# Kernel optimization log

Hardware: AMD Instinct MI355X
Metric: run time of the kernel (lower is better)

The kernel has to match this reference:

```python
import jax, jax.numpy as jnp
import numpy as np

TW = 25; HID = 128; LAYERS = 6; SPATIAL = 1; NVAR = 1
TMAX = 4.0; TMIN = 0.0; RES_T = 250.0; DOM = 16.0
N = 65536; B = 8; E = 393216
EPS = 1e-5


def swish(x):
    return x * jax.nn.sigmoid(x)


def _forward(u, x_pos, t_pos, variables,
             emb_w1, emb_b1, emb_w2, emb_b2,
             m1_w, m1_b, m2_w, m2_b,
             u1_w, u1_b, u2_w, u2_b,
             c1_w, c1_b, c2_w, c2_b,
             edge_index, batch):
    t_norm = t_pos / TMAX                       # [N]
    pos = x_pos / DOM                           # [N, 1] normalized by domain extent
    node_in = jnp.concatenate([u, pos, t_norm[:, None], variables], axis=-1)
    f = swish(node_in @ emb_w1 + emb_b1)
    f = swish(f @ emb_w2 + emb_b2)              # [N, HID]

    var_all = jnp.concatenate([t_norm[:, None], variables], axis=-1)  # [N, NVAR+1]
    src, dst = edge_index[0], edge_index[1]     # PyG: x_j = x[src], x_i = x[dst]
    du = u[dst] - u[src]                        # [E, TW]
    dp = pos[dst] - pos[src]                    # [E, SPATIAL]
    v_i = var_all[dst]                          # [E, NVAR+1]

    ones_e = jnp.ones((E,), f.dtype)
    deg = jnp.maximum(jax.ops.segment_sum(ones_e, dst, num_segments=N), 1.0)
    ones_n = jnp.ones((N,), f.dtype)
    gcount = jnp.maximum(jax.ops.segment_sum(ones_n, batch, num_segments=B), 1.0)

    for l in range(LAYERS):
        # message: concat(x_i, x_j, u_i-u_j, pos_i-pos_j, vars_i) -> 2-layer MLP
        m = jnp.concatenate([f[dst], f[src], du, dp, v_i], axis=-1)  # [E, 284]
        m = swish(m @ m1_w[l] + m1_b[l])
        m = swish(m @ m2_w[l] + m2_b[l])
        agg = jax.ops.segment_sum(m, dst, num_segments=N) / deg[:, None]  # mean aggr
        # update: concat(x, message, vars) -> 2-layer MLP, residual (in==out)
        h = jnp.concatenate([f, agg, var_all], axis=-1)  # [N, 258]
        h = swish(h @ u1_w[l] + u1_b[l])
        h = swish(h @ u2_w[l] + u2_b[l])
        h = f + h
        # InstanceNorm over nodes within each graph, per feature (no affine)
        mean = jax.ops.segment_sum(h, batch, num_segments=B) / gcount[:, None]
        var = jax.ops.segment_sum(h * h, batch, num_segments=B) / gcount[:, None] - mean * mean
        f = (h - mean[batch]) * jax.lax.rsqrt(var[batch] + EPS)

    # output CNN head over feature axis: [N, 1, HID] -> [N, 1, TW]
    y = jax.lax.conv_general_dilated(f[:, None, :], c1_w, (3,), 'VALID',
                                     dimension_numbers=('NCH', 'OIH', 'NCH'))
    y = swish(y + c1_b[None, :, None])
    y = jax.lax.conv_general_dilated(y, c2_w, (1,), 'VALID',
                                     dimension_numbers=('NCH', 'OIH', 'NCH'))
    diff = y[:, 0, :] + c2_b[0]                 # [N, TW]

    dt = jnp.cumsum(jnp.full((TW,), (TMAX - TMIN) / RES_T, dtype=f.dtype))
    out = u[:, -1][:, None] + dt[None, :] * diff
    return out


def setup_inputs() -> dict:
    key = jax.random.key(0)
    keys = iter(jax.random.split(key, 128))

    def lin(i, o):
        s = 1.0 / np.sqrt(i)
        w = jax.random.uniform(next(keys), (i, o), jnp.float32, -s, s)
        b = jax.random.uniform(next(keys), (o,), jnp.float32, -s, s)
        return w, b

    def stacked(i, o):
        ws, bs = zip(*[lin(i, o) for _ in range(LAYERS)])
        return jnp.stack(ws), jnp.stack(bs)

    def conv(o, i, k):
        s = 1.0 / np.sqrt(i * k)
        w = jax.random.uniform(next(keys), (o, i, k), jnp.float32, -s, s)
        b = jax.random.uniform(next(keys), (o,), jnp.float32, -s, s)
        return w, b

    emb_w1, emb_b1 = lin(TW + SPATIAL + 1 + NVAR, HID)
    emb_w2, emb_b2 = lin(HID, HID)
    m1_w, m1_b = stacked(2 * HID + TW + SPATIAL + NVAR + 1, HID)
    m2_w, m2_b = stacked(HID, HID)
    u1_w, u1_b = stacked(2 * HID + NVAR + 1, HID)
    u2_w, u2_b = stacked(HID, HID)
    c1_w, c1_b = conv(8, 1, 16)
    c2_w, c2_b = conv(1, 8, 14)

    u = jax.random.normal(next(keys), (N, TW), jnp.float32)
    x_pos = jax.random.uniform(next(keys), (N, SPATIAL), jnp.float32) * DOM
    t_pos = jax.random.uniform(next(keys), (N,), jnp.float32) * TMAX
    variables = jax.random.normal(next(keys), (N, NVAR), jnp.float32)
    edge_index = jax.random.randint(next(keys), (2, E), 0, N, jnp.int32)
    batch = jnp.sort(jax.random.randint(next(keys), (N,), 0, B, jnp.int32))

    return {'u': u, 'x_pos': x_pos, 't_pos': t_pos, 'variables': variables,
            'edge_index': edge_index, 'batch': batch,
            'emb_w1': emb_w1, 'emb_b1': emb_b1, 'emb_w2': emb_w2, 'emb_b2': emb_b2,
            'm1_w': m1_w, 'm1_b': m1_b, 'm2_w': m2_w, 'm2_b': m2_b,
            'u1_w': u1_w, 'u1_b': u1_b, 'u2_w': u2_w, 'u2_b': u2_b,
            'c1_w': c1_w, 'c1_b': c1_b, 'c2_w': c2_w, 'c2_b': c2_b}


def reference(u, x_pos, t_pos, variables, edge_index, batch,
              emb_w1, emb_b1, emb_w2, emb_b2,
              m1_w, m1_b, m2_w, m2_b,
              u1_w, u1_b, u2_w, u2_b,
              c1_w, c1_b, c2_w, c2_b):
    return _forward(u, x_pos, t_pos, variables,
                    emb_w1, emb_b1, emb_w2, emb_b2,
                    m1_w, m1_b, m2_w, m2_b,
                    u1_w, u1_b, u2_w, u2_b,
                    c1_w, c1_b, c2_w, c2_b,
                    edge_index, batch)
```

## Files before the change

kernel.cpp:

```cpp
#include <hip/hip_runtime.h>
#include <hip/hip_bf16.h>

#define N_NODES 65536
#define N_EDGES 393216
#define NB 8
#define HID 128
#define TW 25
#define LAYERS 6
#define BGRAPH 8
#define EPSF 1e-5f
#define TILE_E 128

typedef __attribute__((ext_vector_type(8))) short bf16x8;
typedef __attribute__((ext_vector_type(4))) float f32x4;

__device__ __forceinline__ float swishf(float x) {
    float den = 1.0f + __expf(-x);
    float r;
    asm("v_rcp_f32 %0, %1" : "=v"(r) : "v"(den));
    return x * r;
}

__device__ __forceinline__ unsigned short f2bf(float x) {
    unsigned int u = __float_as_uint(x);
    u += 0x7fffu + ((u >> 16) & 1u);
    return (unsigned short)(u >> 16);
}

__device__ __forceinline__ unsigned int cvtpk2bf(float lo, float hi) {
    unsigned int r;
    asm("v_cvt_pk_bf16_f32 %0, %1, %2" : "=v"(r) : "v"(lo), "v"(hi));
    return r;
}

__device__ __forceinline__ unsigned short f2bf_rne(float x) {
    unsigned int r;
    asm("v_cvt_pk_bf16_f32 %0, %1, %2" : "=v"(r) : "v"(x), "v"(x));
    return (unsigned short)r;
}

__device__ __forceinline__ float bf2f(unsigned short v) {
    return __uint_as_float(((unsigned int)v) << 16);
}

__global__ void gcount_kernel(const int* __restrict__ batch, float* __restrict__ gcount) {
    int b = threadIdx.x;
    if (b >= BGRAPH) return;
    auto lb = [&](int key) {
        int lo = 0, hi = N_NODES;
        while (lo < hi) { int mid = (lo + hi) >> 1; if (batch[mid] < key) lo = mid + 1; else hi = mid; }
        return lo;
    };
    int c = lb(b + 1) - lb(b);
    gcount[b] = c > 0 ? (float)c : 1.0f;
}

__global__ void count_kernel(const int* __restrict__ ei, int* __restrict__ cnt) {
    int e = blockIdx.x * 256 + threadIdx.x;
    if (e < N_EDGES) atomicAdd(&cnt[ei[N_EDGES + e]], 1);
}

__global__ __launch_bounds__(256) void block_sum_kernel(const int* __restrict__ cnt, int* __restrict__ bsum) {
    __shared__ int s[256];
    int t = threadIdx.x;
    s[t] = cnt[blockIdx.x * 256 + t];
    __syncthreads();
    for (int st = 128; st > 0; st >>= 1) {
        if (t < st) s[t] += s[t + st];
        __syncthreads();
    }
    if (t == 0) bsum[blockIdx.x] = s[0];
}

__global__ __launch_bounds__(256) void scan_bsum_kernel(const int* __restrict__ bsum, int* __restrict__ bpref) {
    __shared__ int s[256];
    int t = threadIdx.x;
    int orig = bsum[t];
    s[t] = orig;
    __syncthreads();
    for (int st = 1; st < 256; st <<= 1) {
        int v = (t >= st) ? s[t - st] : 0;
        __syncthreads();
        s[t] += v;
        __syncthreads();
    }
    bpref[t] = s[t] - orig;
}

__global__ __launch_bounds__(256) void offsets_kernel(const int* __restrict__ cnt, const int* __restrict__ bpref,
                                                      int* __restrict__ cursor) {
    __shared__ int s[256];
    int t = threadIdx.x;
    int base = blockIdx.x * 256;
    int orig = cnt[base + t];
    s[t] = orig;
    __syncthreads();
    for (int st = 1; st < 256; st <<= 1) {
        int v = (t >= st) ? s[t - st] : 0;
        __syncthreads();
        s[t] += v;
        __syncthreads();
    }
    cursor[base + t] = s[t] - orig + bpref[blockIdx.x];
}

__global__ void scatter_kernel(const int* __restrict__ ei, int* __restrict__ cursor,
                               int* __restrict__ src_s, int* __restrict__ dst_s) {
    int e = blockIdx.x * 256 + threadIdx.x;
    if (e >= N_EDGES) return;
    int d = ei[N_EDGES + e];
    int pos = atomicAdd(&cursor[d], 1);
    src_s[pos] = ei[e];
    dst_s[pos] = d;
}

__global__ void w2bf_kernel(const float* __restrict__ m2_w, unsigned short* __restrict__ W2T) {
    int idx = blockIdx.x * 256 + threadIdx.x;
    int l = idx >> 14;
    int rem = idx & 16383;
    int n = rem >> 7, k = rem & 127;
    W2T[idx] = f2bf(m2_w[l * 16384 + k * HID + n]);
}

__global__ void w1t_kernel(const float* __restrict__ m1_w, unsigned short* __restrict__ wAB) {
    int idx = blockIdx.x * 256 + threadIdx.x;
    int l = idx / (2 * 128 * 160);
    int rem = idx % (2 * 128 * 160);
    int pass = rem / (128 * 160);
    int o = (rem % (128 * 160)) / 160;
    int k = rem % 160;
    const float* M = m1_w + (size_t)l * 284 * 128;
    float v;
    if (k < 128) {
        v = M[(pass ? 128 + k : k) * 128 + o];
    } else {
        int ku = k - 128;
        if (ku < 25) v = M[(256 + ku) * 128 + o];
        else if (ku == 25) v = M[281 * 128 + o];
        else if (ku == 26) v = M[282 * 128 + o];
        else if (ku == 27) v = M[283 * 128 + o];
        else v = 0.0f;
        if (pass) v = (ku <= 25) ? -v : 0.0f;
    }
    wAB[idx] = f2bf(v);
}

__global__ void u1t_kernel(const float* __restrict__ u1_w, unsigned short* __restrict__ U1T) {
    int idx = blockIdx.x * 256 + threadIdx.x;
    int l = idx >> 15;
    int o = (idx >> 8) & 127;
    int k = idx & 255;
    U1T[idx] = f2bf(u1_w[(size_t)l * 258 * 128 + k * 128 + o]);
}

__global__ void u2t_kernel(const float* __restrict__ u2_w, unsigned short* __restrict__ U2T) {
    int idx = blockIdx.x * 256 + threadIdx.x;
    int l = idx >> 14;
    int o = (idx >> 7) & 127;
    int k = idx & 127;
    U2T[idx] = f2bf(u2_w[(size_t)l * 16384 + k * 128 + o]);
}

__global__ void wemb_kernel(const float* __restrict__ ew1, const float* __restrict__ ew2,
                            unsigned short* __restrict__ we1T, unsigned short* __restrict__ we2T) {
    int idx = blockIdx.x * 256 + threadIdx.x;
    if (idx < 4096) {
        int o = idx >> 5, k = idx & 31;
        we1T[idx] = f2bf(k < 28 ? ew1[k * HID + o] : 0.0f);
    } else {
        int j = idx - 4096;
        int o = j >> 7, k = j & 127;
        we2T[j] = f2bf(ew2[k * HID + o]);
    }
}

__global__ void xin_kernel(const float* __restrict__ u, const float* __restrict__ xpos,
                           const float* __restrict__ tpos, const float* __restrict__ vars,
                           unsigned short* __restrict__ xin) {
    int idx = blockIdx.x * 256 + threadIdx.x;
    int n = idx >> 5, k = idx & 31;
    float v;
    if (k < 25) v = u[n * TW + k];
    else if (k == 25) v = xpos[n] * (1.0f / 16.0f);
    else if (k == 26) v = tpos[n] * 0.25f;
    else if (k == 27) v = vars[n];
    else v = 0.0f;
    xin[idx] = f2bf(v);
}

__device__ __forceinline__ void abv_chunk(
    const bf16x8 (&afr)[2][5], int nb, int lr, int lk, int colbase,
    const unsigned short* __restrict__ Wp, const float* __restrict__ b1,
    unsigned short* __restrict__ Op)
{
    f32x4 acc[2][2];
    #pragma unroll
    for (int rt = 0; rt < 2; ++rt)
        #pragma unroll
        for (int cf2 = 0; cf2 < 2; ++cf2)
            acc[rt][cf2] = (f32x4){0.0f, 0.0f, 0.0f, 0.0f};
    #pragma unroll
    for (int cf2 = 0; cf2 < 2; ++cf2) {
        const unsigned short* wrow = Wp + (colbase + cf2 * 16 + lr) * 160 + lk * 8;
        #pragma unroll
        for (int ks = 0; ks < 5; ++ks) {
            bf16x8 bfr = *reinterpret_cast<const bf16x8*>(wrow + ks * 32);
            acc[0][cf2] = __builtin_amdgcn_mfma_f32_16x16x32_bf16(afr[0][ks], bfr, acc[0][cf2], 0, 0, 0);
            acc[1][cf2] = __builtin_amdgcn_mfma_f32_16x16x32_bf16(afr[1][ks], bfr, acc[1][cf2], 0, 0, 0);
        }
    }
    #pragma unroll
    for (int cf2 = 0; cf2 < 2; ++cf2) {
        int col = colbase + cf2 * 16 + lr;
        float bb = b1 ? b1[col] : 0.0f;
        #pragma unroll
        for (int rt = 0; rt < 2; ++rt) {
            #pragma unroll
            for (int j = 0; j < 4; ++j) {
                int row = nb + rt * 16 + lk * 4 + j;
                Op[(size_t)row * HID + col] = f2bf_rne(acc[rt][cf2][j] + bb);
            }
        }
    }
}

__global__ __launch_bounds__(256) void emb_abv_kernel(
    const unsigned short* __restrict__ xin_bf,
    const unsigned short* __restrict__ we1T, const float* __restrict__ eb1,
    const unsigned short* __restrict__ we2T, const float* __restrict__ eb2,
    const unsigned short* __restrict__ wA, const unsigned short* __restrict__ wB,
    const float* __restrict__ b1,
    unsigned short* __restrict__ f_bf,
    unsigned short* __restrict__ A_bf, unsigned short* __restrict__ Bv_bf)
{
    __shared__ unsigned short q_lds[4 * 32 * HID];
    const int tid = threadIdx.x;
    const int w = tid >> 6, l = tid & 63;
    const int lr = l & 15, lk = l >> 4;
    const int nb = blockIdx.x * 128 + w * 32;
    char* qbase = reinterpret_cast<char*>(q_lds) + w * 8192;

    bf16x8 xfr[2];
    #pragma unroll
    for (int rt = 0; rt < 2; ++rt)
        xfr[rt] = *reinterpret_cast<const bf16x8*>(xin_bf + (size_t)(nb + rt * 16 + lr) * 32 + lk * 8);

    #pragma unroll 1
    for (int cc = 0; cc < 4; ++cc) {
        f32x4 acc1[2][2];
        #pragma unroll
        for (int rt = 0; rt < 2; ++rt)
            #pragma unroll
            for (int cf2 = 0; cf2 < 2; ++cf2)
                acc1[rt][cf2] = (f32x4){0.0f, 0.0f, 0.0f, 0.0f};
        #pragma unroll
        for (int cf2 = 0; cf2 < 2; ++cf2) {
            bf16x8 bfr = *reinterpret_cast<const bf16x8*>(we1T + ((cc * 2 + cf2) * 16 + lr) * 32 + lk * 8);
            acc1[0][cf2] = __builtin_amdgcn_mfma_f32_16x16x32_bf16(xfr[0], bfr, acc1[0][cf2], 0, 0, 0);
            acc1[1][cf2] = __builtin_amdgcn_mfma_f32_16x16x32_bf16(xfr[1], bfr, acc1[1][cf2], 0, 0, 0);
        }
        #pragma unroll
        for (int cf2 = 0; cf2 < 2; ++cf2) {
            int col = (cc * 2 + cf2) * 16 + lr;
            float bb = eb1[col];
            #pragma unroll
            for (int rt = 0; rt < 2; ++rt)
                #pragma unroll
                for (int j = 0; j < 4; ++j) {
                    float qv = swishf(acc1[rt][cf2][j] + bb);
                    int rloc = rt * 16 + lk * 4 + j;
                    *reinterpret_cast<unsigned short*>(qbase + rloc * 256 + ((col * 2) ^ ((rloc & 7) << 4))) = f2bf_rne(qv);
                }
        }
    }

    __shared__ unsigned short f_lds2[4 * 32 * HID];
    char* fbase = reinterpret_cast<char*>(f_lds2) + w * 8192;
    #pragma unroll 1
    for (int cc = 0; cc < 4; ++cc) {
        f32x4 acc2[2][2];
        #pragma unroll
        for (int rt = 0; rt < 2; ++rt)
            #pragma unroll
            for (int cf2 = 0; cf2 < 2; ++cf2)
                acc2[rt][cf2] = (f32x4){0.0f, 0.0f, 0.0f, 0.0f};
        #pragma unroll
        for (int ks = 0; ks < 4; ++ks) {
            bf16x8 afrq[2];
            #pragma unroll
            for (int rt = 0; rt < 2; ++rt) {
                int rloc = rt * 16 + lr;
                afrq[rt] = *reinterpret_cast<const bf16x8*>(qbase + rloc * 256 + ((ks * 64 + lk * 16) ^ ((rloc & 7) << 4)));
            }
            #pragma unroll
            for (int cf2 = 0; cf2 < 2; ++cf2) {
                bf16x8 bfr = *reinterpret_cast<const bf16x8*>(we2T + ((cc * 2 + cf2) * 16 + lr) * HID + ks * 32 + lk * 8);
                acc2[0][cf2] = __builtin_amdgcn_mfma_f32_16x16x32_bf16(afrq[0], bfr, acc2[0][cf2], 0, 0, 0);
                acc2[1][cf2] = __builtin_amdgcn_mfma_f32_16x16x32_bf16(afrq[1], bfr, acc2[1][cf2], 0, 0, 0);
            }
        }
        #pragma unroll
        for (int cf2 = 0; cf2 < 2; ++cf2) {
            int col = (cc * 2 + cf2) * 16 + lr;
            float bb = eb2[col];
            #pragma unroll
            for (int rt = 0; rt < 2; ++rt)
                #pragma unroll
                for (int j = 0; j < 4; ++j) {
                    float fv = swishf(acc2[rt][cf2][j] + bb);
                    unsigned short fb = f2bf_rne(fv);
                    int rloc = rt * 16 + lk * 4 + j;
                    f_bf[(size_t)(nb + rloc) * HID + col] = fb;
                    *reinterpret_cast<unsigned short*>(fbase + rloc * 256 + ((col * 2) ^ ((rloc & 7) << 4))) = fb;
                }
        }
    }

    bf16x8 afr[2][5];
    #pragma unroll
    for (int rt = 0; rt < 2; ++rt) {
        int rloc = rt * 16 + lr;
        #pragma unroll
        for (int ks = 0; ks < 4; ++ks)
            afr[rt][ks] = *reinterpret_cast<const bf16x8*>(fbase + rloc * 256 + ((ks * 64 + lk * 16) ^ ((rloc & 7) << 4)));
        afr[rt][4] = xfr[rt];
    }
    #pragma unroll 1
    for (int cc = 0; cc < 4; ++cc) abv_chunk(afr, nb, lr, lk, cc * 32, wA, b1, A_bf);
    #pragma unroll 1
    for (int cc = 0; cc < 4; ++cc) abv_chunk(afr, nb, lr, lk, cc * 32, wB, nullptr, Bv_bf);
}

__global__ __launch_bounds__(256) void norm_abv_kernel(
    const unsigned short* __restrict__ h, const int* __restrict__ batch,
    const float* __restrict__ dsum, const float* __restrict__ dsq,
    const float* __restrict__ gcount,
    const unsigned short* __restrict__ xin_bf,
    const unsigned short* __restrict__ wA, const unsigned short* __restrict__ wB,
    const float* __restrict__ b1,
    unsigned short* __restrict__ f_bf,
    unsigned short* __restrict__ A_bf, unsigned short* __restrict__ Bv_bf)
{
    __shared__ unsigned short f_lds[32 * HID];
    const int tid = threadIdx.x;
    const int w = tid >> 6, l = tid & 63;
    const int lr = l & 15, lk = l >> 4;
    const int nb = blockIdx.x * 32;

    {
        const int ks = w;
        const int c0 = ks * 32 + lk * 8;
        #pragma unroll
        for (int rt = 0; rt < 2; ++rt) {
            int row = nb + rt * 16 + lr;
            int b = batch[row];
            float inv = 1.0f / gcount[b];
            uint4 hv4 = *reinterpret_cast<const uint4*>(h + (size_t)row * HID + c0);
            unsigned int hw[4] = {hv4.x, hv4.y, hv4.z, hv4.w};
            float4 s0 = *reinterpret_cast<const float4*>(dsum + b * HID + c0);
            float4 s1 = *reinterpret_cast<const float4*>(dsum + b * HID + c0 + 4);
            float4 q0 = *reinterpret_cast<const float4*>(dsq + b * HID + c0);
            float4 q1 = *reinterpret_cast<const float4*>(dsq + b * HID + c0 + 4);
            float o[8];
            #pragma unroll
            for (int i = 0; i < 8; ++i) {
                float hx = (i & 1) ? __uint_as_float(hw[i >> 1] & 0xffff0000u)
                                   : __uint_as_float(hw[i >> 1] << 16);
                float sm = (i < 4) ? reinterpret_cast<const float*>(&s0)[i] : reinterpret_cast<const float*>(&s1)[i - 4];
                float sq = (i < 4) ? reinterpret_cast<const float*>(&q0)[i] : reinterpret_cast<const float*>(&q1)[i - 4];
                float mean = sm * inv;
                float var = sq * inv - mean * mean;
                o[i] = (hx - mean) * rsqrtf(var + EPSF);
            }
            uint4 t;
            t.x = cvtpk2bf(o[0], o[1]);
            t.y = cvtpk2bf(o[2], o[3]);
            t.z = cvtpk2bf(o[4], o[5]);
            t.w = cvtpk2bf(o[6], o[7]);
            *reinterpret_cast<uint4*>(f_bf + (size_t)row * HID + c0) = t;
            int rloc = rt * 16 + lr;
            *reinterpret_cast<uint4*>(reinterpret_cast<char*>(f_lds) + rloc * 256 + ((c0 * 2) ^ ((rloc & 7) << 4))) = t;
        }
    }
    __syncthreads();

    bf16x8 afr[2][5];
    #pragma unroll
    for (int rt = 0; rt < 2; ++rt) {
        int rloc = rt * 16 + lr;
        #pragma unroll
        for (int ks = 0; ks < 4; ++ks)
            afr[rt][ks] = *reinterpret_cast<const bf16x8*>(
                reinterpret_cast<const char*>(f_lds) + rloc * 256 + ((ks * 64 + lk * 16) ^ ((rloc & 7) << 4)));
        afr[rt][4] = *reinterpret_cast<const bf16x8*>(xin_bf + (size_t)(nb + rt * 16 + lr) * 32 + lk * 8);
    }
    abv_chunk(afr, nb, lr, lk, w * 32, wA, b1, A_bf);
    abv_chunk(afr, nb, lr, lk, w * 32, wB, nullptr, Bv_bf);
}

__global__ __launch_bounds__(256) void edge_mfma_kernel(
    const int* __restrict__ src_s, const int* __restrict__ dst_s,
    const unsigned short* __restrict__ A_bf, const unsigned short* __restrict__ Bv_bf,
    const unsigned short* __restrict__ W2T, const float* __restrict__ b2,
    float* __restrict__ agg)
{
    const int tid = threadIdx.x;
    const int w = tid >> 6, l = tid & 63;
    const int lr = l & 15, lk = l >> 4;
    const int e0 = blockIdx.x * TILE_E + w * 32;

    bf16x8 afr[2][4];
    #pragma unroll
    for (int rt = 0; rt < 2; ++rt) {
        int e = e0 + ((lr >> 2) << 3) + rt * 4 + (lr & 3);
        int dn = dst_s[e], sn = src_s[e];
        const unsigned short* ap = A_bf + (size_t)dn * HID + lk * 8;
        const unsigned short* bp = Bv_bf + (size_t)sn * HID + lk * 8;
        #pragma unroll
        for (int ks = 0; ks < 4; ++ks) {
            uint4 av = *reinterpret_cast<const uint4*>(ap + ks * 32);
            uint4 bv = *reinterpret_cast<const uint4*>(bp + ks * 32);
            auto proc = [](unsigned int aw, unsigned int bw) -> unsigned int {
                float a0 = __uint_as_float(aw << 16), a1 = __uint_as_float(aw & 0xffff0000u);
                float b0 = __uint_as_float(bw << 16), b1 = __uint_as_float(bw & 0xffff0000u);
                return cvtpk2bf(swishf(a0 + b0), swishf(a1 + b1));
            };
            union { bf16x8 v; unsigned int u[4]; } t;
            t.u[0] = proc(av.x, bv.x);
            t.u[1] = proc(av.y, bv.y);
            t.u[2] = proc(av.z, bv.z);
            t.u[3] = proc(av.w, bv.w);
            afr[rt][ks] = t.v;
        }
    }

    const int ebase = e0 + lk * 8;
    int4 dA4 = *reinterpret_cast<const int4*>(dst_s + ebase);
    int4 dB4 = *reinterpret_cast<const int4*>(dst_s + ebase + 4);
    int d[8] = {dA4.x, dA4.y, dA4.z, dA4.w, dB4.x, dB4.y, dB4.z, dB4.w};
    bool sm[7];
    int roff[8];
    #pragma unroll
    for (int m = 0; m < 7; ++m) sm[m] = (d[m + 1] == d[m]);
    #pragma unroll
    for (int m = 0; m < 8; ++m) roff[m] = d[m] * HID;

    #pragma unroll 1
    for (int cc = 0; cc < 4; ++cc) {
        f32x4 acc[2][2];
        #pragma unroll
        for (int rt = 0; rt < 2; ++rt)
            #pragma unroll
            for (int cf2 = 0; cf2 < 2; ++cf2)
                acc[rt][cf2] = (f32x4){0.0f, 0.0f, 0.0f, 0.0f};
        #pragma unroll
        for (int cf2 = 0; cf2 < 2; ++cf2) {
            const unsigned short* wrow = W2T + ((cc * 2 + cf2) * 16 + lr) * HID + lk * 8;
            #pragma unroll
            for (int ks = 0; ks < 4; ++ks) {
                bf16x8 bfr = *reinterpret_cast<const bf16x8*>(wrow + ks * 32);
                acc[0][cf2] = __builtin_amdgcn_mfma_f32_16x16x32_bf16(afr[0][ks], bfr, acc[0][cf2], 0, 0, 0);
                acc[1][cf2] = __builtin_amdgcn_mfma_f32_16x16x32_bf16(afr[1][ks], bfr, acc[1][cf2], 0, 0, 0);
            }
        }
        #pragma unroll
        for (int cf2 = 0; cf2 < 2; ++cf2) {
            int col = (cc * 2 + cf2) * 16 + lr;
            float bias = b2[col];
            float v[8];
            #pragma unroll
            for (int m = 0; m < 8; ++m) v[m] = swishf(acc[m >> 2][cf2][m & 3] + bias);
            float run = v[0];
            #pragma unroll
            for (int m = 1; m < 8; ++m) {
                if (sm[m - 1]) run += v[m];
                else { atomicAdd(&agg[(size_t)roff[m - 1] + col], run); run = v[m]; }
            }
            atomicAdd(&agg[(size_t)roff[7] + col], run);
        }
    }
}

__global__ __launch_bounds__(256) void update_mfma_kernel(
    const unsigned short* __restrict__ f_bf, float* __restrict__ agg,
    const int* __restrict__ cnt,
    const float* __restrict__ tpos, const float* __restrict__ vars,
    const int* __restrict__ batch,
    const unsigned short* __restrict__ U1T, const float* __restrict__ u1tv,
    const float* __restrict__ b1, const unsigned short* __restrict__ U2T,
    const float* __restrict__ b2, unsigned short* __restrict__ h,
    float* __restrict__ dsum, float* __restrict__ dsq)
{
    __shared__ unsigned short q_lds[32 * HID];
    const int tid = threadIdx.x;
    const int w = tid >> 6, l = tid & 63;
    const int lr = l & 15, lk = l >> 4;
    const int nb = blockIdx.x * 32;

    float invd[2];
    #pragma unroll
    for (int rt = 0; rt < 2; ++rt) {
        int c = cnt[nb + rt * 16 + lr];
        invd[rt] = 1.0f / (float)(c > 0 ? c : 1);
    }
    float tn[2][4], vn[2][4];
    #pragma unroll
    for (int rt = 0; rt < 2; ++rt)
        #pragma unroll
        for (int j = 0; j < 4; ++j) {
            int row = nb + rt * 16 + lk * 4 + j;
            tn[rt][j] = tpos[row] * 0.25f;
            vn[rt][j] = vars[row];
        }

    {
        f32x4 acc[2][2];
        #pragma unroll
        for (int rt = 0; rt < 2; ++rt)
            #pragma unroll
            for (int cf2 = 0; cf2 < 2; ++cf2)
                acc[rt][cf2] = (f32x4){0.0f, 0.0f, 0.0f, 0.0f};
        #pragma unroll
        for (int ks = 0; ks < 8; ++ks) {
            bf16x8 afr[2];
            #pragma unroll
            for (int rt = 0; rt < 2; ++rt) {
                int row = nb + rt * 16 + lr;
                if (ks < 4) {
                    afr[rt] = *reinterpret_cast<const bf16x8*>(f_bf + (size_t)row * HID + ks * 32 + lk * 8);
                } else {
                    const float* ap = agg + (size_t)row * HID + (ks - 4) * 32 + lk * 8;
                    float4 a0 = *reinterpret_cast<const float4*>(ap);
                    float4 a1 = *reinterpret_cast<const float4*>(ap + 4);
                    float iv = invd[rt];
                    union { bf16x8 v; unsigned int u[4]; } t;
                    t.u[0] = cvtpk2bf(a0.x * iv, a0.y * iv);
                    t.u[1] = cvtpk2bf(a0.z * iv, a0.w * iv);
                    t.u[2] = cvtpk2bf(a1.x * iv, a1.y * iv);
                    t.u[3] = cvtpk2bf(a1.z * iv, a1.w * iv);
                    afr[rt] = t.v;
                }
            }
            #pragma unroll
            for (int cf2 = 0; cf2 < 2; ++cf2) {
                bf16x8 bfr = *reinterpret_cast<const bf16x8*>(U1T + ((w * 2 + cf2) * 16 + lr) * 256 + ks * 32 + lk * 8);
                acc[0][cf2] = __builtin_amdgcn_mfma_f32_16x16x32_bf16(afr[0], bfr, acc[0][cf2], 0, 0, 0);
                acc[1][cf2] = __builtin_amdgcn_mfma_f32_16x16x32_bf16(afr[1], bfr, acc[1][cf2], 0, 0, 0);
            }
        }
        #pragma unroll
        for (int cf2 = 0; cf2 < 2; ++cf2) {
            int col = w * 32 + cf2 * 16 + lr;
            float bb = b1[col], wt = u1tv[col], wv = u1tv[HID + col];
            #pragma unroll
            for (int rt = 0; rt < 2; ++rt)
                #pragma unroll
                for (int j = 0; j < 4; ++j) {
                    float qv = swishf(acc[rt][cf2][j] + bb + tn[rt][j] * wt + vn[rt][j] * wv);
                    int rloc = rt * 16 + lk * 4 + j;
                    *reinterpret_cast<unsigned short*>(reinterpret_cast<char*>(q_lds) + rloc * 256 + ((col * 2) ^ ((rloc & 7) << 4))) = f2bf_rne(qv);
                }
        }
    }
    __syncthreads();

    {
        #pragma unroll
        for (int i = 0; i < 4; ++i) {
            int q = tid + i * 256;
            int r = q >> 5, cb = q & 31;
            float4 z = {0.0f, 0.0f, 0.0f, 0.0f};
            *reinterpret_cast<float4*>(agg + (size_t)(nb + r) * HID + cb * 4) = z;
        }
    }

    const int bfirst = batch[nb];
    const bool uni = (bfirst == batch[nb + 31]);
    {
        f32x4 acc2[2][2];
        #pragma unroll
        for (int rt = 0; rt < 2; ++rt)
            #pragma unroll
            for (int cf2 = 0; cf2 < 2; ++cf2)
                acc2[rt][cf2] = (f32x4){0.0f, 0.0f, 0.0f, 0.0f};
        #pragma unroll
        for (int ks = 0; ks < 4; ++ks) {
            bf16x8 afr[2];
            #pragma unroll
            for (int rt = 0; rt < 2; ++rt) {
                int rloc = rt * 16 + lr;
                afr[rt] = *reinterpret_cast<const bf16x8*>(
                    reinterpret_cast<const char*>(q_lds) + rloc * 256 + ((ks * 64 + lk * 16) ^ ((rloc & 7) << 4)));
            }
            #pragma unroll
            for (int cf2 = 0; cf2 < 2; ++cf2) {
                bf16x8 bfr = *reinterpret_cast<const bf16x8*>(U2T + ((w * 2 + cf2) * 16 + lr) * HID + ks * 32 + lk * 8);
                acc2[0][cf2] = __builtin_amdgcn_mfma_f32_16x16x32_bf16(afr[0], bfr, acc2[0][cf2], 0, 0, 0);
                acc2[1][cf2] = __builtin_amdgcn_mfma_f32_16x16x32_bf16(afr[1], bfr, acc2[1][cf2], 0, 0, 0);
            }
        }
        #pragma unroll
        for (int cf2 = 0; cf2 < 2; ++cf2) {
            int col = w * 32 + cf2 * 16 + lr;
            float bb = b2[col];
            float s = 0.0f, s2 = 0.0f;
            #pragma unroll
            for (int rt = 0; rt < 2; ++rt)
                #pragma unroll
                for (int j = 0; j < 4; ++j) {
                    int row = nb + rt * 16 + lk * 4 + j;
                    float fres = bf2f(f_bf[(size_t)row * HID + col]);
                    float hv = fres + swishf(acc2[rt][cf2][j] + bb);
                    unsigned short hb = f2bf_rne(hv);
                    h[(size_t)row * HID + col] = hb;
                    float hvr = bf2f(hb);
                    if (uni) { s += hvr; s2 += hvr * hvr; }
                    else {
                        int b = batch[row];
                        atomicAdd(&dsum[b * HID + col], hvr);
                        atomicAdd(&dsq[b * HID + col], hvr * hvr);
                    }
                }
            if (uni) {
                s += __shfl_xor(s, 16); s += __shfl_xor(s, 32);
                s2 += __shfl_xor(s2, 16); s2 += __shfl_xor(s2, 32);
                if (lk == 0) {
                    atomicAdd(&dsum[bfirst * HID + col], s);
                    atomicAdd(&dsq[bfirst * HID + col], s2);
                }
            }
        }
    }
}

__global__ __launch_bounds__(256) void head_kernel(
    const unsigned short* __restrict__ h, const int* __restrict__ batch,
    const float* __restrict__ dsum, const float* __restrict__ dsq,
    const float* __restrict__ gcount,
    const float* __restrict__ u,
    const float* __restrict__ c1w, const float* __restrict__ c1b,
    const float* __restrict__ c2w, const float* __restrict__ c2b,
    float* __restrict__ out)
{
    __shared__ float fs[16][HID];
    __shared__ float y1[16][8][40];
    const int tid = threadIdx.x;
    const int n0 = blockIdx.x * 16;
    {
        int node = tid >> 4, cb = tid & 15;
        int n = n0 + node;
        int b = batch[n];
        float inv = 1.0f / gcount[b];
        int c0 = cb * 8;
        uint4 v = *reinterpret_cast<const uint4*>(h + (size_t)n * HID + c0);
        unsigned int wv[4] = {v.x, v.y, v.z, v.w};
        #pragma unroll
        for (int i = 0; i < 8; ++i) {
            float hx = (i & 1) ? __uint_as_float(wv[i >> 1] & 0xffff0000u)
                               : __uint_as_float(wv[i >> 1] << 16);
            float mean = dsum[b * HID + c0 + i] * inv;
            float var = dsq[b * HID + c0 + i] * inv - mean * mean;
            fs[node][c0 + i] = (hx - mean) * rsqrtf(var + EPSF);
        }
    }
    __syncthreads();
    {
        const int node = tid >> 4;
        const int rem = tid & 15;
        const int o = rem >> 1;
        const int ph = rem & 1;
        const float cb = c1b[o];
        float wk[16];
        #pragma unroll
        for (int k = 0; k < 16; ++k) wk[k] = c1w[o * 16 + k];
        for (int p = ph * 19; p < ph * 19 + 19; ++p) {
            float acc = cb;
            #pragma unroll
            for (int k = 0; k < 16; ++k) acc += fs[node][p * 3 + k] * wk[k];
            y1[node][o][p] = swishf(acc);
        }
    }
    __syncthreads();
    const float cb2 = c2b[0];
    #pragma unroll
    for (int pass = 0; pass < 2; ++pass) {
        int unit = tid + pass * 256;
        if (unit < 16 * TW) {
            int node = unit / TW, t = unit % TW;
            float acc = cb2;
            #pragma unroll
            for (int o = 0; o < 8; ++o)
                #pragma unroll
                for (int k = 0; k < 14; ++k)
                    acc += y1[node][o][t + k] * c2w[o * 14 + k];
            int n = n0 + node;
            out[n * TW + t] = u[n * TW + (TW - 1)] + (0.016f * (float)(t + 1)) * acc;
        }
    }
}

extern "C" void kernel_launch(void* const* d_in, const int* in_sizes, int n_in,
                              void* d_out, int out_size, void* d_ws, size_t ws_size,
                              hipStream_t stream)
{
    (void)in_sizes; (void)n_in; (void)out_size; (void)ws_size;
    const float* u      = (const float*)d_in[0];
    const float* xpos   = (const float*)d_in[1];
    const float* tpos   = (const float*)d_in[2];
    const float* vars   = (const float*)d_in[3];
    const int*   ei     = (const int*)d_in[4];
    const int*   batch  = (const int*)d_in[5];
    const float* emb_w1 = (const float*)d_in[6];
    const float* emb_b1 = (const float*)d_in[7];
    const float* emb_w2 = (const float*)d_in[8];
    const float* emb_b2 = (const float*)d_in[9];
    const float* m1_w   = (const float*)d_in[10];
    const float* m1_b   = (const float*)d_in[11];
    const float* m2_w   = (const float*)d_in[12];
    const float* m2_b   = (const float*)d_in[13];
    const float* u1_w   = (const float*)d_in[14];
    const float* u1_b   = (const float*)d_in[15];
    const float* u2_w   = (const float*)d_in[16];
    const float* u2_b   = (const float*)d_in[17];
    const float* c1w    = (const float*)d_in[18];
    const float* c1b    = (const float*)d_in[19];
    const float* c2w    = (const float*)d_in[20];
    const float* c2b    = (const float*)d_in[21];
    float* out = (float*)d_out;

    char* ws = (char*)d_ws;
    const size_t fbytes = (size_t)N_NODES * HID * sizeof(float);
    float* agg    = (float*)(ws);
    char*  p      = ws + fbytes;
    unsigned short* h_bf   = (unsigned short*)p;  p += (size_t)N_NODES * HID * 2;
    unsigned short* A_bf   = (unsigned short*)p;  p += (size_t)N_NODES * HID * 2;
    unsigned short* Bv_bf  = (unsigned short*)p;  p += (size_t)N_NODES * HID * 2;
    unsigned short* f_bf   = (unsigned short*)p;  p += (size_t)N_NODES * HID * 2;
    unsigned short* xin_bf = (unsigned short*)p;  p += (size_t)N_NODES * 32 * 2;
    int* cnt      = (int*)p;               p += (size_t)N_NODES * 4;
    int* cursor   = (int*)p;               p += (size_t)N_NODES * 4;
    int* src_s    = (int*)p;               p += (size_t)N_EDGES * 4;
    int* dst_s    = (int*)p;               p += (size_t)N_EDGES * 4;
    int* bsum     = (int*)p;               p += 256 * 4;
    int* bpref    = (int*)p;               p += 256 * 4;
    float* dsumL  = (float*)p;             p += (size_t)LAYERS * BGRAPH * HID * 4;
    float* dsqL   = (float*)p;             p += (size_t)LAYERS * BGRAPH * HID * 4;
    float* gcount = (float*)p;             p += BGRAPH * 4;
    unsigned short* W2T  = (unsigned short*)p;  p += (size_t)LAYERS * HID * HID * 2;
    unsigned short* wAB  = (unsigned short*)p;  p += (size_t)LAYERS * 2 * 128 * 160 * 2;
    unsigned short* U1T  = (unsigned short*)p;  p += (size_t)LAYERS * 128 * 256 * 2;
    unsigned short* U2T  = (unsigned short*)p;  p += (size_t)LAYERS * 128 * 128 * 2;
    unsigned short* we1T = (unsigned short*)p;  p += 128 * 32 * 2;
    unsigned short* we2T = (unsigned short*)p;  p += 128 * 128 * 2;

    hipMemsetAsync(cnt, 0, (size_t)N_NODES * 4, stream);
    count_kernel<<<N_EDGES / 256, 256, 0, stream>>>(ei, cnt);
    block_sum_kernel<<<N_NODES / 256, 256, 0, stream>>>(cnt, bsum);
    scan_bsum_kernel<<<1, 256, 0, stream>>>(bsum, bpref);
    offsets_kernel<<<N_NODES / 256, 256, 0, stream>>>(cnt, bpref, cursor);
    scatter_kernel<<<N_EDGES / 256, 256, 0, stream>>>(ei, cursor, src_s, dst_s);

    w2bf_kernel<<<LAYERS * HID * HID / 256, 256, 0, stream>>>(m2_w, W2T);
    w1t_kernel<<<LAYERS * 2 * 128 * 160 / 256, 256, 0, stream>>>(m1_w, wAB);
    u1t_kernel<<<LAYERS * 128 * 256 / 256, 256, 0, stream>>>(u1_w, U1T);
    u2t_kernel<<<LAYERS * 128 * 128 / 256, 256, 0, stream>>>(u2_w, U2T);
    wemb_kernel<<<80, 256, 0, stream>>>(emb_w1, emb_w2, we1T, we2T);
    xin_kernel<<<N_NODES * 32 / 256, 256, 0, stream>>>(u, xpos, tpos, vars, xin_bf);
    gcount_kernel<<<1, 64, 0, stream>>>(batch, gcount);
    hipMemsetAsync(dsumL, 0, (size_t)2 * LAYERS * BGRAPH * HID * 4, stream);
    hipMemsetAsync(agg, 0, fbytes, stream);

    emb_abv_kernel<<<N_NODES / 128, 256, 0, stream>>>(
        xin_bf, we1T, emb_b1, we2T, emb_b2,
        wAB, wAB + 128 * 160, m1_b, f_bf, A_bf, Bv_bf);

    for (int l = 0; l < LAYERS; ++l) {
        edge_mfma_kernel<<<N_EDGES / TILE_E, 256, 0, stream>>>(
            src_s, dst_s, A_bf, Bv_bf, W2T + (size_t)l * HID * HID,
            m2_b + (size_t)l * HID, agg);
        update_mfma_kernel<<<N_NODES / 32, 256, 0, stream>>>(
            f_bf, agg, cnt, tpos, vars, batch,
            U1T + (size_t)l * 128 * 256,
            u1_w + (size_t)l * 258 * 128 + 256 * 128,
            u1_b + (size_t)l * HID,
            U2T + (size_t)l * 128 * 128,
            u2_b + (size_t)l * HID, h_bf,
            dsumL + (size_t)l * BGRAPH * HID, dsqL + (size_t)l * BGRAPH * HID);
        if (l < LAYERS - 1) {
            norm_abv_kernel<<<N_NODES / 32, 256, 0, stream>>>(
                h_bf, batch, dsumL + (size_t)l * BGRAPH * HID, dsqL + (size_t)l * BGRAPH * HID,
                gcount, xin_bf,
                wAB + (size_t)(l + 1) * 2 * 128 * 160,
                wAB + (size_t)(l + 1) * 2 * 128 * 160 + 128 * 160,
                m1_b + (size_t)(l + 1) * HID,
                f_bf, A_bf, Bv_bf);
        }
    }
    head_kernel<<<N_NODES / 16, 256, 0, stream>>>(
        h_bf, batch, dsumL + (size_t)(LAYERS - 1) * BGRAPH * HID,
        dsqL + (size_t)(LAYERS - 1) * BGRAPH * HID, gcount,
        u, c1w, c1b, c2w, c2b, out);
}
```

Measured before the change: 1.142 ms.

## Process two edge tiles per wave, prefetching second gather during first compute

Each wave in the edge kernel now handles two 32-edge chunks. The raw A/B gathers for the second chunk are issued before the MFMA and atomic stage of the first chunk runs, so memory latency can overlap with compute, and the grid is halved to match. The cost is more registers held live (the raw uint4 buffers), which may lower occupancy.

```diff
diff --git a/kernel.cpp b/kernel.cpp
--- a/kernel.cpp
+++ b/kernel.cpp
@@ -9,7 +9,6 @@
 #define LAYERS 6
 #define BGRAPH 8
 #define EPSF 1e-5f
-#define TILE_E 128
 
 typedef __attribute__((ext_vector_type(8))) short bf16x8;
 typedef __attribute__((ext_vector_type(4))) float f32x4;
@@ -398,43 +397,54 @@
     abv_chunk(afr, nb, lr, lk, w * 32, wB, nullptr, Bv_bf);
 }
 
-__global__ __launch_bounds__(256) void edge_mfma_kernel(
+__device__ __forceinline__ void edge_gather_raw(
+    int eg, int lr, int lk,
     const int* __restrict__ src_s, const int* __restrict__ dst_s,
     const unsigned short* __restrict__ A_bf, const unsigned short* __restrict__ Bv_bf,
-    const unsigned short* __restrict__ W2T, const float* __restrict__ b2,
-    float* __restrict__ agg)
-{
-    const int tid = threadIdx.x;
-    const int w = tid >> 6, l = tid & 63;
-    const int lr = l & 15, lk = l >> 4;
-    const int e0 = blockIdx.x * TILE_E + w * 32;
-
-    bf16x8 afr[2][4];
+    uint4 (&av)[2][4], uint4 (&bv)[2][4])
+{
     #pragma unroll
     for (int rt = 0; rt < 2; ++rt) {
-        int e = e0 + ((lr >> 2) << 3) + rt * 4 + (lr & 3);
+        int e = eg + ((lr >> 2) << 3) + rt * 4 + (lr & 3);
         int dn = dst_s[e], sn = src_s[e];
         const unsigned short* ap = A_bf + (size_t)dn * HID + lk * 8;
         const unsigned short* bp = Bv_bf + (size_t)sn * HID + lk * 8;
         #pragma unroll
         for (int ks = 0; ks < 4; ++ks) {
-            uint4 av = *reinterpret_cast<const uint4*>(ap + ks * 32);
-            uint4 bv = *reinterpret_cast<const uint4*>(bp + ks * 32);
+            av[rt][ks] = *reinterpret_cast<const uint4*>(ap + ks * 32);
+            bv[rt][ks] = *reinterpret_cast<const uint4*>(bp + ks * 32);
+        }
+    }
+}
+
+__device__ __forceinline__ void edge_convert(
+    const uint4 (&av)[2][4], const uint4 (&bv)[2][4], bf16x8 (&afr)[2][4])
+{
+    #pragma unroll
+    for (int rt = 0; rt < 2; ++rt)
+        #pragma unroll
+        for (int ks = 0; ks < 4; ++ks) {
             auto proc = [](unsigned int aw, unsigned int bw) -> unsigned int {
                 float a0 = __uint_as_float(aw << 16), a1 = __uint_as_float(aw & 0xffff0000u);
                 float b0 = __uint_as_float(bw << 16), b1 = __uint_as_float(bw & 0xffff0000u);
                 return cvtpk2bf(swishf(a0 + b0), swishf(a1 + b1));
             };
             union { bf16x8 v; unsigned int u[4]; } t;
-            t.u[0] = proc(av.x, bv.x);
-            t.u[1] = proc(av.y, bv.y);
-            t.u[2] = proc(av.z, bv.z);
-            t.u[3] = proc(av.w, bv.w);
+            t.u[0] = proc(av[rt][ks].x, bv[rt][ks].x);
+            t.u[1] = proc(av[rt][ks].y, bv[rt][ks].y);
+            t.u[2] = proc(av[rt][ks].z, bv[rt][ks].z);
+            t.u[3] = proc(av[rt][ks].w, bv[rt][ks].w);
             afr[rt][ks] = t.v;
         }
-    }
-
-    const int ebase = e0 + lk * 8;
+}
+
+__device__ __forceinline__ void edge_compute(
+    int eg, int lr, int lk, const bf16x8 (&afr)[2][4],
+    const int* __restrict__ dst_s,
+    const unsigned short* __restrict__ W2T, const float* __restrict__ b2,
+    float* __restrict__ agg)
+{
+    const int ebase = eg + lk * 8;
     int4 dA4 = *reinterpret_cast<const int4*>(dst_s + ebase);
     int4 dB4 = *reinterpret_cast<const int4*>(dst_s + ebase + 4);
     int d[8] = {dA4.x, dA4.y, dA4.z, dA4.w, dB4.x, dB4.y, dB4.z, dB4.w};
@@ -479,6 +489,32 @@
             atomicAdd(&agg[(size_t)roff[7] + col], run);
         }
     }
+}
+
+__global__ __launch_bounds__(256) void edge_mfma_kernel(
+    const int* __restrict__ src_s, const int* __restrict__ dst_s,
+    const unsigned short* __restrict__ A_bf, const unsigned short* __restrict__ Bv_bf,
+    const unsigned short* __restrict__ W2T, const float* __restrict__ b2,
+    float* __restrict__ agg)
+{
+    const int tid = threadIdx.x;
+    const int w = tid >> 6, l = tid & 63;
+    const int lr = l & 15, lk = l >> 4;
+    const int e0 = blockIdx.x * 256 + w * 64;
+
+    uint4 av0[2][4], bv0[2][4];
+    edge_gather_raw(e0, lr, lk, src_s, dst_s, A_bf, Bv_bf, av0, bv0);
+    bf16x8 afr0[2][4];
+    edge_convert(av0, bv0, afr0);
+
+    uint4 av1[2][4], bv1[2][4];
+    edge_gather_raw(e0 + 32, lr, lk, src_s, dst_s, A_bf, Bv_bf, av1, bv1);
+
+    edge_compute(e0, lr, lk, afr0, dst_s, W2T, b2, agg);
+
+    bf16x8 afr1[2][4];
+    edge_convert(av1, bv1, afr1);
+    edge_compute(e0 + 32, lr, lk, afr1, dst_s, W2T, b2, agg);
 }
 
 __global__ __launch_bounds__(256) void update_mfma_kernel(
@@ -775,7 +811,7 @@
         wAB, wAB + 128 * 160, m1_b, f_bf, A_bf, Bv_bf);
 
     for (int l = 0; l < LAYERS; ++l) {
-        edge_mfma_kernel<<<N_EDGES / TILE_E, 256, 0, stream>>>(
+        edge_mfma_kernel<<<N_EDGES / 256, 256, 0, stream>>>(
             src_s, dst_s, A_bf, Bv_bf, W2T + (size_t)l * HID * HID,
             m2_b + (size_t)l * HID, agg);
         update_mfma_kernel<<<N_NODES / 32, 256, 0, stream>>>(
```

Measured after the change: 1.256 ms. 1.1x slower.
